# Optimization experiments

Hardware: AMD Instinct MI355X
Metric: run time of the kernel (lower is better)

The kernel has to match this reference:

```python
import jax, jax.numpy as jnp
import numpy as np

UNITS = 2048
D_IN = 96
BATCH = 64
T = 512
C_IN = 10        # connectivity_input: nnz per input-kernel row
C_REC = 10       # connectivity_recurrent: nnz per recurrent-kernel column
INPUT_SCALING = 1.0
SPECTRAL_RADIUS = 0.99
LEAKY = 1.0


def setup_inputs() -> dict:
    rng = np.random.default_rng(0)
    # --- input kernel: sparse (D_IN, UNITS), C_IN nonzeros per row (COO) ---
    krows = np.repeat(np.arange(D_IN), C_IN).astype(np.int32)                 # [D_IN*C_IN]
    kcols = np.stack([rng.choice(UNITS, size=C_IN, replace=False)
                      for _ in range(D_IN)]).reshape(-1).astype(np.int32)
    kvals = (2.0 * (2.0 * rng.random(D_IN * C_IN) - 1.0)).astype(np.float32) * np.float32(INPUT_SCALING)
    # --- recurrent kernel: sparse (UNITS, UNITS), C_REC nonzeros per column ---
    # rec_idx[i, j] = source row feeding output unit (column) i
    rec_idx = np.stack([rng.choice(UNITS, size=C_REC, replace=False)
                        for _ in range(UNITS)]).astype(np.int32)              # [UNITS, C_REC]
    rec_vals = (2.0 * (2.0 * rng.random((UNITS, C_REC)) - 1.0)).astype(np.float32)
    # spectral-radius normalization via exact eigenvalues (matches tf.linalg.eig path, leaky==1)
    W = np.zeros((UNITS, UNITS), np.float32)
    W[rec_idx.reshape(-1), np.repeat(np.arange(UNITS), C_REC)] = rec_vals.reshape(-1)
    rho = np.abs(np.linalg.eigvals(W)).max()
    rec_vals = rec_vals * np.float32(SPECTRAL_RADIUS / rho)
    # --- bias ---
    bias = (2.0 * rng.random(UNITS) - 1.0).astype(np.float32) * np.float32(INPUT_SCALING)
    key = jax.random.key(0)
    inputs = jax.random.normal(key, (BATCH, T, D_IN), dtype=jnp.float32)
    state0 = jnp.zeros((BATCH, UNITS), dtype=jnp.float32)
    return {
        "inputs": inputs,
        "state0": state0,
        "kernel_vals": jnp.asarray(kvals),
        "rec_vals": jnp.asarray(rec_vals),
        "bias": jnp.asarray(bias),
        "kernel_rows": jnp.asarray(krows),
        "kernel_cols": jnp.asarray(kcols),
        "rec_idx": jnp.asarray(rec_idx),
    }


def reference(inputs, state0, kernel_vals, rec_vals, bias, kernel_rows, kernel_cols, rec_idx):
    units = bias.shape[0]

    def step(h, x_t):                                     # h: [B, units], x_t: [B, D_IN]
        # input_part = x_t @ kernel (sparse COO, fixed degree per row)
        contrib = x_t[:, kernel_rows] * kernel_vals       # [B, nnz_in]
        input_part = jax.ops.segment_sum(contrib.T, kernel_cols, num_segments=units).T  # [B, units]
        # state_part = h @ W (fixed C_REC sources per output unit -> gather+reduce)
        state_part = jnp.einsum('bnc,nc->bn', h[:, rec_idx], rec_vals)  # [B, units]
        h_new = h * (1.0 - LEAKY) + jnp.tanh(input_part + bias + state_part) * LEAKY
        return h_new, h_new

    _, ys = jax.lax.scan(step, state0, jnp.swapaxes(inputs, 0, 1))  # ys: [T, B, units]
    return jnp.swapaxes(ys, 0, 1)                                   # [B, T, units]
```

## Files before the change

### kernel.cpp

```cpp
#include <hip/hip_runtime.h>

namespace {
constexpr int UNITS = 2048;
constexpr int D_IN  = 96;
constexpr int BATCH = 64;
constexpr int T     = 512;
constexpr int NNZ   = 960;
constexpr int C_REC = 10;
constexpr int NT    = 1024;
constexpr int NCOPY = 4;

constexpr int HA = 0;
constexpr int HB = 32768;
constexpr int IA = 65536;
constexpr int IB = 73728;
constexpr int LDS_BYTES = 81920;

constexpr int OFFS_OFS = 0;
constexpr int WTAB_OFS = 20 * NT * 4;
constexpr int WS_NEED  = 40 * NT * 4;
}

typedef float f32x2 __attribute__((ext_vector_type(2)));
typedef float f32x4 __attribute__((ext_vector_type(4)));

__device__ __forceinline__ void bar_lds() {
  asm volatile("s_waitcnt lgkmcnt(0)\n\ts_barrier" ::: "memory");
}

__device__ __forceinline__ float fast_tanh(float x) {
  float e = __expf(2.0f * x);
  return 1.0f - __fdividef(2.0f, e + 1.0f);
}

__global__ __launch_bounds__(64) void prep_sched(
    const int* __restrict__ ridx, const float* __restrict__ rvals,
    int* __restrict__ offs, float* __restrict__ wtab)
{
  const int w = blockIdx.x, l = threadIdx.x;
  __shared__ int           sidx[128 * C_REC];
  __shared__ float         sval[128 * C_REC];
  __shared__ unsigned char hist[20][32];
  for (int i = l; i < 128 * C_REC; i += 64) {
    sidx[i] = ridx[w * 128 * C_REC + i];
    sval[i] = rvals[w * 128 * C_REC + i];
  }
  if (l < 32)
    for (int s = 0; s < 20; ++s) hist[s][l] = 0;
  __syncthreads();

  unsigned remA = 0x3FF, remB = 0x3FF;
  for (int step = 0; step < 20 + 63; ++step) {
    const int s = step - l;
    if (s >= 0 && s < 20) {
      const int p  = s & 1;
      unsigned& rem = p ? remB : remA;
      const int ul = 2 * l + p;
      int beste = 0, bestc = 0, bestload = 999, bestidx = 0;
      for (int e = 0; e < C_REC; ++e) {
        if (!((rem >> e) & 1)) continue;
        int idx = sidx[ul * C_REC + e];
        for (int c = 0; c < NCOPY; ++c) {
          int ld = hist[s][(idx + 8 * c) & 31];
          if (ld < bestload) { bestload = ld; beste = e; bestc = c; bestidx = idx; }
        }
      }
      hist[s][(bestidx + 8 * bestc) & 31] = (unsigned char)(bestload + 1);
      rem &= ~(1u << beste);
      const int tid = w * 64 + l;
      offs[s * NT + tid] = bestc * 8192 + ((bestidx + 8 * bestc) & 2047) * 4;
      wtab[s * NT + tid] = sval[ul * C_REC + beste];
    }
    __syncthreads();
  }
}

#define RDECL(k)                                                               \
  const int   oA##k = PERM ? offs[(2*(k)) * NT + tid]                          \
                           : ridx[u0 * C_REC + (k)] * 4;                       \
  const float wA##k = PERM ? wtab[(2*(k)) * NT + tid]                          \
                           : rvals[u0 * C_REC + (k)];                          \
  const int   oB##k = PERM ? offs[(2*(k)+1) * NT + tid]                        \
                           : ridx[(u0 + 1) * C_REC + (k)] * 4;                 \
  const float wB##k = PERM ? wtab[(2*(k)+1) * NT + tid]                        \
                           : rvals[(u0 + 1) * C_REC + (k)];

#define GAT(HC, k)                                                             \
  s0 += *(const float*)(smem + (HC) + oA##k) * wA##k;                          \
  s1 += *(const float*)(smem + (HC) + oB##k) * wB##k;

#define STEP(HC, HN, IR, IW, DO_SCATTER, TSTEP)                                \
  {                                                                            \
    f32x2 in2 = *(f32x2*)(smem + (IR) + tid * 8);                              \
    *(f32x2*)(smem + (IR) + tid * 8) = (f32x2){0.f, 0.f};                      \
    float s0 = in2.x + bias2.x;                                                \
    float s1 = in2.y + bias2.y;                                                \
    GAT(HC, 0) GAT(HC, 1) GAT(HC, 2) GAT(HC, 3) GAT(HC, 4)                     \
    GAT(HC, 5) GAT(HC, 6) GAT(HC, 7) GAT(HC, 8) GAT(HC, 9)                     \
    if ((DO_SCATTER) && e0) atomicAdd((float*)(smem + (IW) + kcb), xn * kv);   \
    f32x2 hh = {fast_tanh(s0), fast_tanh(s1)};                                 \
    *(f32x2*)(smem + (HN) + pb0) = hh;                                         \
    *(f32x2*)(smem + (HN) + pb1) = hh;                                         \
    *(f32x2*)(smem + (HN) + pb2) = hh;                                         \
    *(f32x2*)(smem + (HN) + pb3) = hh;                                         \
    __builtin_nontemporal_store(hh, outp + (size_t)(TSTEP) * (UNITS / 2));     \
    if (e0) {                                                                  \
      int tnx = (TSTEP) + 2 < T ? (TSTEP) + 2 : T - 1;                         \
      xn = xin[tnx * D_IN + r0];                                               \
    }                                                                          \
    bar_lds();                                                                 \
  }

template <bool PERM>
__global__ __launch_bounds__(NT, 4) void reservoir_kernel(
    const float* __restrict__ inputs, const float* __restrict__ state0,
    const float* __restrict__ kvals,  const float* __restrict__ rvals,
    const float* __restrict__ bias,   const int* __restrict__ krows,
    const int* __restrict__ kcols,    const int* __restrict__ ridx,
    const int* __restrict__ offs,     const float* __restrict__ wtab,
    float* __restrict__ out)
{
  __shared__ __align__(16) char smem[LDS_BYTES];
  const int tid = threadIdx.x;
  const int b   = blockIdx.x;
  const int u0  = 2 * tid;

  const int pb0 =         u0 * 4;
  const int pb1 = 8192  + ((u0 + 8)  & 2047) * 4;
  const int pb2 = 16384 + ((u0 + 16) & 2047) * 4;
  const int pb3 = 24576 + ((u0 + 24) & 2047) * 4;

  *(f32x2*)(smem + IA + tid * 8) = (f32x2){0.f, 0.f};
  *(f32x2*)(smem + IB + tid * 8) = (f32x2){0.f, 0.f};
  f32x2 h0 = *(const f32x2*)(state0 + b * UNITS + u0);
  *(f32x2*)(smem + HA + pb0) = h0;
  *(f32x2*)(smem + HA + pb1) = h0;
  *(f32x2*)(smem + HA + pb2) = h0;
  *(f32x2*)(smem + HA + pb3) = h0;

  RDECL(0) RDECL(1) RDECL(2) RDECL(3) RDECL(4)
  RDECL(5) RDECL(6) RDECL(7) RDECL(8) RDECL(9)

  const f32x2 bias2 = *(const f32x2*)(bias + u0);

  const bool e0 = tid < NNZ;
  const int   r0  = e0 ? krows[tid] : 0;
  const int   kcb = e0 ? kcols[tid] * 4 : 0;
  const float kv  = e0 ? kvals[tid] : 0.f;

  const float* xin  = inputs + (size_t)b * (T * D_IN);
  f32x2*       outp = (f32x2*)out + (size_t)b * (T * (UNITS / 2)) + tid;

  float xn = e0 ? xin[r0] : 0.f;
  __syncthreads();
  if (e0) atomicAdd((float*)(smem + IA + kcb), xn * kv);
  if (e0) xn = xin[D_IN + r0];
  bar_lds();

#pragma unroll 1
  for (int ts = 0; ts < T; ts += 2) {
    STEP(HA, HB, IA, IB, true,         ts);
    STEP(HB, HA, IB, IA, (ts + 2) < T, ts + 1);
  }
}

extern "C" void kernel_launch(void* const* d_in, const int* in_sizes, int n_in,
                              void* d_out, int out_size, void* d_ws, size_t ws_size,
                              hipStream_t stream) {
  const float* inputs = (const float*)d_in[0];
  const float* state0 = (const float*)d_in[1];
  const float* kvals  = (const float*)d_in[2];
  const float* rvals  = (const float*)d_in[3];
  const float* bias   = (const float*)d_in[4];
  const int*   krows  = (const int*)d_in[5];
  const int*   kcols  = (const int*)d_in[6];
  const int*   ridx   = (const int*)d_in[7];

  int*   offs = (int*)((char*)d_ws + OFFS_OFS);
  float* wtab = (float*)((char*)d_ws + WTAB_OFS);

  if (ws_size >= (size_t)WS_NEED) {
    prep_sched<<<dim3(16), dim3(64), 0, stream>>>(ridx, rvals, offs, wtab);
    reservoir_kernel<true><<<dim3(BATCH), dim3(NT), 0, stream>>>(
        inputs, state0, kvals, rvals, bias, krows, kcols, ridx, offs, wtab,
        (float*)d_out);
  } else {
    reservoir_kernel<false><<<dim3(BATCH), dim3(NT), 0, stream>>>(
        inputs, state0, kvals, rvals, bias, krows, kcols, ridx, offs, wtab,
        (float*)d_out);
  }
}
```

Baseline: 1.254 ms.

## Cut hidden-state LDS copies from four to two using XOR-swizzled second copy

The hidden state is now mirrored in two LDS copies instead of four, and the second copy uses an XOR swizzle of pair indices in place of a rotation. The prep scheduler is rewritten to place gathers greedily by bank occupancy across only these two copies, using atomics on a per-step histogram. This halves the per-step LDS state writes and the LDS footprint, but gives fewer choices for avoiding bank conflicts on the random gathers, so conflicts may rise.

```diff
diff --git a/kernel.cpp b/kernel.cpp
--- a/kernel.cpp
+++ b/kernel.cpp
@@ -8,13 +8,12 @@
 constexpr int NNZ   = 960;
 constexpr int C_REC = 10;
 constexpr int NT    = 1024;
-constexpr int NCOPY = 4;
 
 constexpr int HA = 0;
-constexpr int HB = 32768;
-constexpr int IA = 65536;
-constexpr int IB = 73728;
-constexpr int LDS_BYTES = 81920;
+constexpr int HB = 16384;
+constexpr int IA = 32768;
+constexpr int IB = 40960;
+constexpr int LDS_BYTES = 49152;
 
 constexpr int OFFS_OFS = 0;
 constexpr int WTAB_OFS = 20 * NT * 4;
@@ -33,44 +32,52 @@
   return 1.0f - __fdividef(2.0f, e + 1.0f);
 }
 
+__device__ __forceinline__ int c1_byte(int idx) {
+  int p = idx >> 1;
+  return 8192 + (2 * (p ^ ((p >> 4) & 15)) + (idx & 1)) * 4;
+}
+
 __global__ __launch_bounds__(64) void prep_sched(
     const int* __restrict__ ridx, const float* __restrict__ rvals,
     int* __restrict__ offs, float* __restrict__ wtab)
 {
   const int w = blockIdx.x, l = threadIdx.x;
-  __shared__ int           sidx[128 * C_REC];
-  __shared__ float         sval[128 * C_REC];
-  __shared__ unsigned char hist[20][32];
+  __shared__ int   sidx[128 * C_REC];
+  __shared__ float sval[128 * C_REC];
+  __shared__ int   hist[32];
   for (int i = l; i < 128 * C_REC; i += 64) {
     sidx[i] = ridx[w * 128 * C_REC + i];
     sval[i] = rvals[w * 128 * C_REC + i];
   }
-  if (l < 32)
-    for (int s = 0; s < 20; ++s) hist[s][l] = 0;
   __syncthreads();
+  const int tidm = w * 64 + l;
+  unsigned rem0 = 0x3FF, rem1 = 0x3FF;
 
-  unsigned remA = 0x3FF, remB = 0x3FF;
-  for (int step = 0; step < 20 + 63; ++step) {
-    const int s = step - l;
-    if (s >= 0 && s < 20) {
-      const int p  = s & 1;
-      unsigned& rem = p ? remB : remA;
-      const int ul = 2 * l + p;
-      int beste = 0, bestc = 0, bestload = 999, bestidx = 0;
-      for (int e = 0; e < C_REC; ++e) {
-        if (!((rem >> e) & 1)) continue;
-        int idx = sidx[ul * C_REC + e];
-        for (int c = 0; c < NCOPY; ++c) {
-          int ld = hist[s][(idx + 8 * c) & 31];
-          if (ld < bestload) { bestload = ld; beste = e; bestc = c; bestidx = idx; }
-        }
-      }
-      hist[s][(bestidx + 8 * bestc) & 31] = (unsigned char)(bestload + 1);
-      rem &= ~(1u << beste);
-      const int tid = w * 64 + l;
-      offs[s * NT + tid] = bestc * 8192 + ((bestidx + 8 * bestc) & 2047) * 4;
-      wtab[s * NT + tid] = sval[ul * C_REC + beste];
+  for (int s = 0; s < 20; ++s) {
+    if (l < 32) hist[l] = 0;
+    __syncthreads();
+    const int p = s & 1;
+    unsigned& rem = p ? rem1 : rem0;
+    const int ul = 2 * l + p;
+    const unsigned m = rem;
+    const int nc = 2 * __popc(m);
+    int pe = -1, pidx = 0, pcp = 0;
+    for (int r = 0; r < 6 && pe < 0; ++r) {
+      const int rr = (r < nc) ? r : (r % nc);
+      const int er = rr >> 1, cp = rr & 1;
+      int cnt = 0, ce = 0;
+#pragma unroll
+      for (int e = 0; e < C_REC; ++e)
+        if ((m >> e) & 1) { if (cnt == er) ce = e; ++cnt; }
+      const int idx  = sidx[ul * C_REC + ce];
+      const int bank = cp ? ((c1_byte(idx) >> 2) & 31) : (idx & 31);
+      const int old  = atomicAdd(&hist[bank], 1);
+      if (old < 2 || r == 5) { pe = ce; pcp = cp; pidx = idx; }
+      else atomicSub(&hist[bank], 1);
     }
+    rem = m & ~(1u << pe);
+    offs[s * NT + tidm] = pcp ? c1_byte(pidx) : pidx * 4;
+    wtab[s * NT + tidm] = sval[ul * C_REC + pe];
     __syncthreads();
   }
 }
@@ -101,8 +108,6 @@
     f32x2 hh = {fast_tanh(s0), fast_tanh(s1)};                                 \
     *(f32x2*)(smem + (HN) + pb0) = hh;                                         \
     *(f32x2*)(smem + (HN) + pb1) = hh;                                         \
-    *(f32x2*)(smem + (HN) + pb2) = hh;                                         \
-    *(f32x2*)(smem + (HN) + pb3) = hh;                                         \
     __builtin_nontemporal_store(hh, outp + (size_t)(TSTEP) * (UNITS / 2));     \
     if (e0) {                                                                  \
       int tnx = (TSTEP) + 2 < T ? (TSTEP) + 2 : T - 1;                         \
@@ -125,18 +130,14 @@
   const int b   = blockIdx.x;
   const int u0  = 2 * tid;
 
-  const int pb0 =         u0 * 4;
-  const int pb1 = 8192  + ((u0 + 8)  & 2047) * 4;
-  const int pb2 = 16384 + ((u0 + 16) & 2047) * 4;
-  const int pb3 = 24576 + ((u0 + 24) & 2047) * 4;
+  const int pb0 = u0 * 4;
+  const int pb1 = 8192 + (tid ^ ((tid >> 4) & 15)) * 8;
 
   *(f32x2*)(smem + IA + tid * 8) = (f32x2){0.f, 0.f};
   *(f32x2*)(smem + IB + tid * 8) = (f32x2){0.f, 0.f};
   f32x2 h0 = *(const f32x2*)(state0 + b * UNITS + u0);
   *(f32x2*)(smem + HA + pb0) = h0;
   *(f32x2*)(smem + HA + pb1) = h0;
-  *(f32x2*)(smem + HA + pb2) = h0;
-  *(f32x2*)(smem + HA + pb3) = h0;
 
   RDECL(0) RDECL(1) RDECL(2) RDECL(3) RDECL(4)
   RDECL(5) RDECL(6) RDECL(7) RDECL(8) RDECL(9)
```

Result: faster. 1.148 ms (-8.4%).
